# Optimization experiments

Measured on AMD Instinct MI355X. Metric: run time of the kernel, lower is better.

## Reference

```python
import jax, jax.numpy as jnp
import numpy as np

N_ACTIONS = 4
HIDDEN = 32

def setup_inputs() -> dict:
    key = jax.random.key(0)
    ks = jax.random.split(key, 8)
    B, T = 2048, 1024
    prev_actions_onehot = jax.random.uniform(ks[0], (B, T, N_ACTIONS), dtype=jnp.float32)
    prev_rewards = jax.random.normal(ks[1], (B, T, 1), dtype=jnp.float32)
    in_dim = N_ACTIONS + 1
    s_ih = 1.0 / np.sqrt(HIDDEN)
    W_ih = jax.random.uniform(ks[2], (HIDDEN, in_dim), jnp.float32, -s_ih, s_ih)
    W_hh = jax.random.uniform(ks[3], (HIDDEN, HIDDEN), jnp.float32, -s_ih, s_ih)
    b_ih = jax.random.uniform(ks[4], (HIDDEN,), jnp.float32, -s_ih, s_ih)
    b_hh = jax.random.uniform(ks[5], (HIDDEN,), jnp.float32, -s_ih, s_ih)
    W_ro = jax.random.uniform(ks[6], (N_ACTIONS, HIDDEN), jnp.float32, -s_ih, s_ih)
    b_ro = jax.random.uniform(ks[7], (N_ACTIONS,), jnp.float32, -s_ih, s_ih)
    return {
        'prev_actions_onehot': prev_actions_onehot,
        'prev_rewards': prev_rewards,
        'W_ih': W_ih, 'W_hh': W_hh, 'b_ih': b_ih, 'b_hh': b_hh,
        'W_ro': W_ro, 'b_ro': b_ro,
    }

def reference(prev_actions_onehot, prev_rewards, W_ih, W_hh, b_ih, b_hh, W_ro, b_ro):
    # x_seq: [B, T, n_actions+1]
    x_seq = jnp.concatenate([prev_actions_onehot, prev_rewards], axis=-1)
    B = x_seq.shape[0]
    # Precompute the input projection for all steps (parallel): [B, T, H]
    x_proj = jnp.einsum('bti,hi->bth', x_seq, W_ih) + b_ih + b_hh
    h0 = jnp.zeros((B, HIDDEN), dtype=x_seq.dtype)

    def step(h, xp_t):
        # xp_t: [B, H] (already contains x@W_ih^T + b_ih + b_hh)
        h_new = jnp.tanh(xp_t + h @ W_hh.T)
        return h_new, h_new

    # scan over time: move T to leading axis
    h_T, hs = jax.lax.scan(step, h0, jnp.swapaxes(x_proj, 0, 1))
    hs = jnp.swapaxes(hs, 0, 1)  # [B, T, H]
    logits_seq = jnp.einsum('bth,ah->bta', hs, W_ro) + b_ro  # [B, T, n_actions]
    return logits_seq, h_T
```

## Files before the change

### kernel.cpp

```cpp
#include <hip/hip_runtime.h>

#define H 32
#define GPB 16

__device__ __forceinline__ float fast_tanh(float x) {
    float e = __builtin_amdgcn_exp2f(x * 2.8853900817779268f);
    float r = __builtin_amdgcn_rcpf(e + 1.0f);
    return fmaf(-2.0f, r, 1.0f);
}

#define QFMA(acc, p, w, q) \
    asm("v_fmac_f32_dpp %0, %1, %2 quad_perm:[" #q "," #q "," #q "," #q "] row_mask:0xf bank_mask:0xf" \
        : "+v"(acc) : "v"(p), "v"(w))

#define MV4(i, pv) \
    QFMA(a0, pv, whh[i],      0); \
    QFMA(a1, pv, whh[8 + i],  1); \
    QFMA(a2, pv, whh[16 + i], 2); \
    QFMA(a3, pv, whh[24 + i], 3)

#define DPPMOV(x, ctrl) \
    __int_as_float(__builtin_amdgcn_update_dpp(0, __float_as_int(x), (ctrl), 0xf, 0xf, true))
#define ROW_SHR1 0x111
#define ROW_SHR2 0x112
#define ROW_SHR4 0x114

#define XP(oh, rwc) fmaf((oh).x, wih0, fmaf((oh).y, wih1, fmaf((oh).z, wih2, \
                     fmaf((oh).w, wih3, fmaf((rwc), wih4, bias)))))

struct F8 { float4 a, b; };

__global__ __launch_bounds__(512, 2) void rnn_fused(
    const float* __restrict__ onehot,
    const float* __restrict__ rewards,
    const float* __restrict__ W_ih,
    const float* __restrict__ W_hh,
    const float* __restrict__ b_ih,
    const float* __restrict__ b_hh,
    const float* __restrict__ W_ro,
    const float* __restrict__ b_ro,
    float* __restrict__ out_logits,
    float* __restrict__ out_hT,
    int T)
{
    const int tid = threadIdx.x;
    const int u   = tid & 31;
    const int wl  = tid & 63;
    const int wv  = tid >> 6;
    const int b   = blockIdx.x * GPB + (tid >> 5);
    const int qp  = u & 3;
    const int r   = u >> 3;
    const bool hi = ((u >> 2) & 1) != 0;
    const bool writer = (u & 7) == 7;

    __shared__ __align__(16) float hbuf[8 * 64];
    float* wptr = &hbuf[wv * 64 + wl];
    const float4* gp = (const float4*)&hbuf[wv * 64 + (wl & 32) + 8 * qp];

    float whh[H];
#pragma unroll
    for (int k = 0; k < 8; ++k) {
        float4 w = *(const float4*)(W_hh + u * H + 4 * k);
        whh[4*k+0] = w.x; whh[4*k+1] = w.y; whh[4*k+2] = w.z; whh[4*k+3] = w.w;
    }
    const float wih0 = W_ih[u*5+0], wih1 = W_ih[u*5+1], wih2 = W_ih[u*5+2],
                wih3 = W_ih[u*5+3], wih4 = W_ih[u*5+4];
    const float bias = b_ih[u] + b_hh[u];
    const float4 wr4 = *(const float4*)(W_ro + r * H + qp * 8 + (hi ? 4 : 0));
    const float bro = b_ro[r];

    const float* oh_ptr = onehot  + (size_t)b * T * 4;
    const float* rw_ptr = rewards + (size_t)b * T;
    float*       lg_ptr = out_logits + (size_t)b * T * 4;

    float4 oh0, oh1, oh2, oh3, rwv;
    float4 qh0, qh1, qh2, qh3, qrw;

    auto loadX = [&](int t) {
        oh0 = *(const float4*)(oh_ptr + (size_t)t * 4);
        oh1 = *(const float4*)(oh_ptr + (size_t)(t + 1) * 4);
        oh2 = *(const float4*)(oh_ptr + (size_t)(t + 2) * 4);
        oh3 = *(const float4*)(oh_ptr + (size_t)(t + 3) * 4);
        rwv = *(const float4*)(rw_ptr + t);
    };
    auto loadY = [&](int t) {
        qh0 = *(const float4*)(oh_ptr + (size_t)t * 4);
        qh1 = *(const float4*)(oh_ptr + (size_t)(t + 1) * 4);
        qh2 = *(const float4*)(oh_ptr + (size_t)(t + 2) * 4);
        qh3 = *(const float4*)(oh_ptr + (size_t)(t + 3) * 4);
        qrw = *(const float4*)(rw_ptr + t);
    };

    float hj = 0.0f;
    F8 pA, pB;

    auto readout = [&](const F8& p, int t) {
        float s0 = hi ? p.b.x : p.a.x;
        float s1 = hi ? p.b.y : p.a.y;
        float s2 = hi ? p.b.z : p.a.z;
        float s3 = hi ? p.b.w : p.a.w;
        float s = fmaf(s3, wr4.w, fmaf(s2, wr4.z, fmaf(s1, wr4.y, s0 * wr4.x)));
        s += DPPMOV(s, ROW_SHR1);
        s += DPPMOV(s, ROW_SHR2);
        s += DPPMOV(s, ROW_SHR4);
        if (writer) lg_ptr[(size_t)t * 4 + r] = s + bro;
    };

    auto step = [&](F8& pN, const F8& pO,
                    const float4& oh, float rwc, int t, bool ro) {
        *wptr = hj;
        pN.a = gp[0];
        pN.b = gp[1];
        if (ro) readout(pO, t - 2);
        const float xp = XP(oh, rwc);
        float a0 = xp, a1 = 0.f, a2 = 0.f, a3 = 0.f;
        MV4(0, pN.a.x); MV4(1, pN.a.y); MV4(2, pN.a.z); MV4(3, pN.a.w);
        MV4(4, pN.b.x); MV4(5, pN.b.y); MV4(6, pN.b.z); MV4(7, pN.b.w);
        hj = fast_tanh((a0 + a1) + (a2 + a3));
    };

    loadX(0);
    loadY(4);
    step(pA, pB, oh0, rwv.x, 0, false);
    step(pB, pA, oh1, rwv.y, 1, false);
    step(pA, pB, oh2, rwv.z, 2, true);
    step(pB, pA, oh3, rwv.w, 3, true);
    loadX(8);
    step(pA, pB, qh0, qrw.x, 4, true);
    step(pB, pA, qh1, qrw.y, 5, true);
    step(pA, pB, qh2, qrw.z, 6, true);
    step(pB, pA, qh3, qrw.w, 7, true);

    for (int tb = 8; tb < T; tb += 8) {
        if (tb + 4 < T) loadY(tb + 4);
        step(pA, pB, oh0, rwv.x, tb + 0, true);
        step(pB, pA, oh1, rwv.y, tb + 1, true);
        step(pA, pB, oh2, rwv.z, tb + 2, true);
        step(pB, pA, oh3, rwv.w, tb + 3, true);
        if (tb + 8 < T) loadX(tb + 8);
        step(pA, pB, qh0, qrw.x, tb + 4, true);
        step(pB, pA, qh1, qrw.y, tb + 5, true);
        step(pA, pB, qh2, qrw.z, tb + 6, true);
        step(pB, pA, qh3, qrw.w, tb + 7, true);
    }

    readout(pB, T - 2);
    *wptr = hj;
    pA.a = gp[0];
    pA.b = gp[1];
    readout(pA, T - 1);
    out_hT[(size_t)b * H + u] = hj;
}

extern "C" void kernel_launch(void* const* d_in, const int* in_sizes, int n_in,
                              void* d_out, int out_size, void* d_ws, size_t ws_size,
                              hipStream_t stream) {
    const float* onehot  = (const float*)d_in[0];
    const float* rewards = (const float*)d_in[1];
    const float* W_ih    = (const float*)d_in[2];
    const float* W_hh    = (const float*)d_in[3];
    const float* b_ih    = (const float*)d_in[4];
    const float* b_hh    = (const float*)d_in[5];
    const float* W_ro    = (const float*)d_in[6];
    const float* b_ro    = (const float*)d_in[7];

    const int T = 1024;
    const int B = in_sizes[1] / T;

    float* out_logits = (float*)d_out;
    float* out_hT     = (float*)d_out + (size_t)B * T * 4;

    dim3 block(512);
    dim3 grid(B / GPB);
    rnn_fused<<<grid, block, 0, stream>>>(onehot, rewards, W_ih, W_hh,
                                          b_ih, b_hh, W_ro, b_ro,
                                          out_logits, out_hT, T);
}
```

Baseline: 368.0 us.

## Replace LDS hidden-state broadcast with DPP rotations and ds_swizzle in RNN step

Each recurrent step no longer writes the hidden state to shared memory and reads it back. It broadcasts h within the 32-lane group using a ds_swizzle across the 16-lane halves plus DPP row-rotate and quad-perm moves, with W_hh pre-permuted per lane to match the rotation order. The readout is folded into the same step, reusing the broadcast values for the previous h and emitting the logit one step later. Block size is halved to 256 threads with launch bounds (256,1). The aim is to cut LDS round-trip latency on the serial critical path, at the cost of more DPP move instructions per step and changed occupancy.

Measured after the change: 342.9 us. -6.8%, faster.

```diff
diff --git a/kernel.cpp b/kernel.cpp
--- a/kernel.cpp
+++ b/kernel.cpp
@@ -1,7 +1,7 @@
 #include <hip/hip_runtime.h>
 
 #define H 32
-#define GPB 16
+#define GPB 8
 
 __device__ __forceinline__ float fast_tanh(float x) {
     float e = __builtin_amdgcn_exp2f(x * 2.8853900817779268f);
@@ -9,28 +9,28 @@
     return fmaf(-2.0f, r, 1.0f);
 }
 
-#define QFMA(acc, p, w, q) \
-    asm("v_fmac_f32_dpp %0, %1, %2 quad_perm:[" #q "," #q "," #q "," #q "] row_mask:0xf bank_mask:0xf" \
-        : "+v"(acc) : "v"(p), "v"(w))
-
-#define MV4(i, pv) \
-    QFMA(a0, pv, whh[i],      0); \
-    QFMA(a1, pv, whh[8 + i],  1); \
-    QFMA(a2, pv, whh[16 + i], 2); \
-    QFMA(a3, pv, whh[24 + i], 3)
-
 #define DPPMOV(x, ctrl) \
     __int_as_float(__builtin_amdgcn_update_dpp(0, __float_as_int(x), (ctrl), 0xf, 0xf, true))
-#define ROW_SHR1 0x111
-#define ROW_SHR2 0x112
-#define ROW_SHR4 0x114
+#define QP0 0x00
+#define QP1 0x55
+#define QP2 0xAA
+#define QP3 0xFF
+#define RR4 0x124
+#define SHR4 0x114
+#define SHR8 0x118
+#define SWZ_X16 0x401F
 
 #define XP(oh, rwc) fmaf((oh).x, wih0, fmaf((oh).y, wih1, fmaf((oh).z, wih2, \
                      fmaf((oh).w, wih3, fmaf((rwc), wih4, bias)))))
 
-struct F8 { float4 a, b; };
+#define STAGE(rr, W, j0) do { \
+    q0 = DPPMOV(rr, QP0); q1 = DPPMOV(rr, QP1); \
+    q2 = DPPMOV(rr, QP2); q3 = DPPMOV(rr, QP3); \
+    a0 = fmaf(q0, W[j0+0], a0); a1 = fmaf(q1, W[j0+1], a1); \
+    a2 = fmaf(q2, W[j0+2], a2); a3 = fmaf(q3, W[j0+3], a3); \
+} while (0)
 
-__global__ __launch_bounds__(512, 2) void rnn_fused(
+__global__ __launch_bounds__(256, 1) void rnn_fused(
     const float* __restrict__ onehot,
     const float* __restrict__ rewards,
     const float* __restrict__ W_ih,
@@ -45,29 +45,27 @@
 {
     const int tid = threadIdx.x;
     const int u   = tid & 31;
-    const int wl  = tid & 63;
-    const int wv  = tid >> 6;
     const int b   = blockIdx.x * GPB + (tid >> 5);
-    const int qp  = u & 3;
-    const int r   = u >> 3;
-    const bool hi = ((u >> 2) & 1) != 0;
-    const bool writer = (u & 7) == 7;
+    const bool wr = (u >= 12) && (u < 16);
 
-    __shared__ __align__(16) float hbuf[8 * 64];
-    float* wptr = &hbuf[wv * 64 + wl];
-    const float4* gp = (const float4*)&hbuf[wv * 64 + (wl & 32) + 8 * qp];
-
-    float whh[H];
-#pragma unroll
-    for (int k = 0; k < 8; ++k) {
-        float4 w = *(const float4*)(W_hh + u * H + 4 * k);
-        whh[4*k+0] = w.x; whh[4*k+1] = w.y; whh[4*k+2] = w.z; whh[4*k+3] = w.w;
+    float wown[16], woth[16];
+    {
+        const int base = u & 16;
+        const int rb   = 4 * ((u >> 2) & 3);
+        #pragma unroll
+        for (int j = 0; j < 16; ++j) {
+            const int s = j >> 2, bq = j & 3;
+            const int kin = (rb + bq - 4 * s) & 15;
+            wown[j] = W_hh[u * H + base + kin];
+            woth[j] = W_hh[u * H + (base ^ 16) + kin];
+        }
     }
     const float wih0 = W_ih[u*5+0], wih1 = W_ih[u*5+1], wih2 = W_ih[u*5+2],
                 wih3 = W_ih[u*5+3], wih4 = W_ih[u*5+4];
     const float bias = b_ih[u] + b_hh[u];
-    const float4 wr4 = *(const float4*)(W_ro + r * H + qp * 8 + (hi ? 4 : 0));
-    const float bro = b_ro[r];
+    const float4 wroq  = *(const float4*)(W_ro + (u & 3) * H + (u & ~3));
+    const float4 wroq2 = *(const float4*)(W_ro + (u & 3) * H + ((u & ~3) ^ 16));
+    const float broz = b_ro[u & 3];
 
     const float* oh_ptr = onehot  + (size_t)b * T * 4;
     const float* rw_ptr = rewards + (size_t)b * T;
@@ -75,7 +73,6 @@
 
     float4 oh0, oh1, oh2, oh3, rwv;
     float4 qh0, qh1, qh2, qh3, qrw;
-
     auto loadX = [&](int t) {
         oh0 = *(const float4*)(oh_ptr + (size_t)t * 4);
         oh1 = *(const float4*)(oh_ptr + (size_t)(t + 1) * 4);
@@ -91,64 +88,87 @@
         qrw = *(const float4*)(rw_ptr + t);
     };
 
-    float hj = 0.0f;
-    F8 pA, pB;
+    float hj;
 
-    auto readout = [&](const F8& p, int t) {
-        float s0 = hi ? p.b.x : p.a.x;
-        float s1 = hi ? p.b.y : p.a.y;
-        float s2 = hi ? p.b.z : p.a.z;
-        float s3 = hi ? p.b.w : p.a.w;
-        float s = fmaf(s3, wr4.w, fmaf(s2, wr4.z, fmaf(s1, wr4.y, s0 * wr4.x)));
-        s += DPPMOV(s, ROW_SHR1);
-        s += DPPMOV(s, ROW_SHR2);
-        s += DPPMOV(s, ROW_SHR4);
-        if (writer) lg_ptr[(size_t)t * 4 + r] = s + bro;
-    };
-
-    auto step = [&](F8& pN, const F8& pO,
-                    const float4& oh, float rwc, int t, bool ro) {
-        *wptr = hj;
-        pN.a = gp[0];
-        pN.b = gp[1];
-        if (ro) readout(pO, t - 2);
-        const float xp = XP(oh, rwc);
-        float a0 = xp, a1 = 0.f, a2 = 0.f, a3 = 0.f;
-        MV4(0, pN.a.x); MV4(1, pN.a.y); MV4(2, pN.a.z); MV4(3, pN.a.w);
-        MV4(4, pN.b.x); MV4(5, pN.b.y); MV4(6, pN.b.z); MV4(7, pN.b.w);
+    auto step = [&](const float4& oh, float rwc, int emit_t) {
+        const float h0 = hj;
+        const int hsb = __builtin_amdgcn_ds_swizzle(__float_as_int(h0), SWZ_X16);
+        float a0 = XP(oh, rwc), a1 = 0.f, a2 = 0.f, a3 = 0.f;
+        float q0, q1, q2, q3;
+        STAGE(h0, wown, 0);
+        float pr = q0 * wroq.x;
+        pr = fmaf(q1, wroq.y, pr);
+        pr = fmaf(q2, wroq.z, pr);
+        pr = fmaf(q3, wroq.w, pr);
+        float r = DPPMOV(h0, RR4);
+        STAGE(r, wown, 4);
+        r = DPPMOV(r, RR4);
+        STAGE(r, wown, 8);
+        r = DPPMOV(r, RR4);
+        STAGE(r, wown, 12);
+        const float hs = __int_as_float(hsb);
+        STAGE(hs, woth, 0);
+        pr = fmaf(q0, wroq2.x, pr);
+        pr = fmaf(q1, wroq2.y, pr);
+        pr = fmaf(q2, wroq2.z, pr);
+        pr = fmaf(q3, wroq2.w, pr);
+        r = DPPMOV(hs, RR4);
+        STAGE(r, woth, 4);
+        r = DPPMOV(r, RR4);
+        STAGE(r, woth, 8);
+        r = DPPMOV(r, RR4);
+        STAGE(r, woth, 12);
+        float t1 = pr + DPPMOV(pr, SHR4);
+        float t2 = t1 + DPPMOV(t1, SHR8);
+        if (wr) lg_ptr[(size_t)emit_t * 4 + (u & 3)] = t2 + broz;
         hj = fast_tanh((a0 + a1) + (a2 + a3));
     };
 
     loadX(0);
     loadY(4);
-    step(pA, pB, oh0, rwv.x, 0, false);
-    step(pB, pA, oh1, rwv.y, 1, false);
-    step(pA, pB, oh2, rwv.z, 2, true);
-    step(pB, pA, oh3, rwv.w, 3, true);
+    hj = fast_tanh(XP(oh0, rwv.x));
+    step(oh1, rwv.y, 0);
+    step(oh2, rwv.z, 1);
+    step(oh3, rwv.w, 2);
     loadX(8);
-    step(pA, pB, qh0, qrw.x, 4, true);
-    step(pB, pA, qh1, qrw.y, 5, true);
-    step(pA, pB, qh2, qrw.z, 6, true);
-    step(pB, pA, qh3, qrw.w, 7, true);
+    step(qh0, qrw.x, 3);
+    step(qh1, qrw.y, 4);
+    step(qh2, qrw.z, 5);
+    step(qh3, qrw.w, 6);
+    loadY(12);
 
     for (int tb = 8; tb < T; tb += 8) {
-        if (tb + 4 < T) loadY(tb + 4);
-        step(pA, pB, oh0, rwv.x, tb + 0, true);
-        step(pB, pA, oh1, rwv.y, tb + 1, true);
-        step(pA, pB, oh2, rwv.z, tb + 2, true);
-        step(pB, pA, oh3, rwv.w, tb + 3, true);
+        step(oh0, rwv.x, tb - 1);
+        step(oh1, rwv.y, tb + 0);
+        step(oh2, rwv.z, tb + 1);
+        step(oh3, rwv.w, tb + 2);
         if (tb + 8 < T) loadX(tb + 8);
-        step(pA, pB, qh0, qrw.x, tb + 4, true);
-        step(pB, pA, qh1, qrw.y, tb + 5, true);
-        step(pA, pB, qh2, qrw.z, tb + 6, true);
-        step(pB, pA, qh3, qrw.w, tb + 7, true);
+        step(qh0, qrw.x, tb + 3);
+        step(qh1, qrw.y, tb + 4);
+        step(qh2, qrw.z, tb + 5);
+        step(qh3, qrw.w, tb + 6);
+        if (tb + 12 < T) loadY(tb + 12);
     }
 
-    readout(pB, T - 2);
-    *wptr = hj;
-    pA.a = gp[0];
-    pA.b = gp[1];
-    readout(pA, T - 1);
+    {
+        const int hsb = __builtin_amdgcn_ds_swizzle(__float_as_int(hj), SWZ_X16);
+        float q0 = DPPMOV(hj, QP0), q1 = DPPMOV(hj, QP1),
+              q2 = DPPMOV(hj, QP2), q3 = DPPMOV(hj, QP3);
+        float pr = q0 * wroq.x;
+        pr = fmaf(q1, wroq.y, pr);
+        pr = fmaf(q2, wroq.z, pr);
+        pr = fmaf(q3, wroq.w, pr);
+        const float hs = __int_as_float(hsb);
+        q0 = DPPMOV(hs, QP0); q1 = DPPMOV(hs, QP1);
+        q2 = DPPMOV(hs, QP2); q3 = DPPMOV(hs, QP3);
+        pr = fmaf(q0, wroq2.x, pr);
+        pr = fmaf(q1, wroq2.y, pr);
+        pr = fmaf(q2, wroq2.z, pr);
+        pr = fmaf(q3, wroq2.w, pr);
+        float t1 = pr + DPPMOV(pr, SHR4);
+        float t2 = t1 + DPPMOV(t1, SHR8);
+        if (wr) lg_ptr[(size_t)(T - 1) * 4 + (u & 3)] = t2 + broz;
+    }
     out_hT[(size_t)b * H + u] = hj;
 }
 
@@ -170,7 +190,7 @@
     float* out_logits = (float*)d_out;
     float* out_hT     = (float*)d_out + (size_t)B * T * 4;
 
-    dim3 block(512);
+    dim3 block(256);
     dim3 grid(B / GPB);
     rnn_fused<<<grid, block, 0, stream>>>(onehot, rewards, W_ih, W_hh,
                                           b_ih, b_hh, W_ro, b_ro,
```
